# Performance work log

Hardware: AMD Instinct MI355X
Metric: run time of the kernel (lower is better)

The kernel has to match this reference:

```python
import jax, jax.numpy as jnp
import numpy as np

NHEAD = 16


def setup_inputs() -> dict:
    key = jax.random.key(0)
    ks = jax.random.split(key, 9)
    d = 1024
    scale = 0.03  # keep projected q,k in a sane range (like trained weights)
    return {
        "x": jax.random.normal(ks[0], (4, 4096, d), jnp.float32),
        "wq": jax.random.normal(ks[1], (d, d), jnp.float32) * scale,
        "bq": jax.random.normal(ks[2], (d,), jnp.float32) * scale,
        "wk": jax.random.normal(ks[3], (d, d), jnp.float32) * scale,
        "bk": jax.random.normal(ks[4], (d,), jnp.float32) * scale,
        "wv": jax.random.normal(ks[5], (d, d), jnp.float32) * scale,
        "bv": jax.random.normal(ks[6], (d,), jnp.float32) * scale,
        "wo": jax.random.normal(ks[7], (d, d), jnp.float32) * scale,
        "bo": jax.random.normal(ks[8], (d,), jnp.float32) * scale,
        "window_size": 128,
    }


def reference(x, wq, bq, wk, bk, wv, bv, wo, bo, window_size):
    B, S, D = x.shape
    H = NHEAD
    Dh = D // H
    w = int(window_size)

    def proj(wm, b):
        # [B,S,D] -> [B,H,S,Dh]
        return (x @ wm.T + b).reshape(B, S, H, Dh).transpose(0, 2, 1, 3)

    q = proj(wq, bq)
    k = proj(wk, bk)
    v = proj(wv, bv)

    # Pad K/V along seq so offset slices are static-size [B,H,S,Dh].
    Kp = jnp.pad(k, ((0, 0), (0, 0), (w, w), (0, 0)))
    Vp = jnp.pad(v, ((0, 0), (0, 0), (w, w), (0, 0)))
    pos = jnp.arange(S)
    inv_sqrt = np.float32(1.0 / np.sqrt(Dh))

    # Faithful to the Triton kernel: a sequential scan over window offsets with a
    # RUNNING max but NO rescaling of the accumulators (the kernel's exact math).
    def step(carry, t):
        m, o_acc, t_acc = carry
        kj = jax.lax.dynamic_slice_in_dim(Kp, t, S, axis=2)  # key at offset t-w
        vj = jax.lax.dynamic_slice_in_dim(Vp, t, S, axis=2)
        s = jnp.einsum("bhsd,bhsd->bhs", q, kj) * inv_sqrt
        j = pos + t - w
        valid = (j >= 0) & (j < S)  # [S], broadcasts over [B,H,S]
        m_new = jnp.where(valid, jnp.maximum(m, s), m)
        p = jnp.exp(jnp.where(valid, s - m_new, -jnp.inf))  # 0 where invalid
        return (m_new, o_acc + p[..., None] * vj, t_acc + p), None

    init = (
        jnp.full((B, H, S), -jnp.inf, dtype=x.dtype),
        jnp.zeros((B, H, S, Dh), dtype=x.dtype),
        jnp.zeros((B, H, S), dtype=x.dtype),
    )
    (m, o_acc, t_acc), _ = jax.lax.scan(step, init, jnp.arange(2 * w + 1))
    o = o_acc / t_acc[..., None]  # [B,H,S,Dh]
    out = o.transpose(0, 2, 1, 3).reshape(B, S, D)
    return out @ wo.T + bo
```

## Files before the change

### kernel.cpp

```cpp
#include <hip/hip_runtime.h>
#include <math.h>

#define S_LEN  4096
#define BATCH  4
#define DMODEL 1024
#define NHEADS 16
#define DHEAD  64
#define WIN    128

typedef _Float16 half8   __attribute__((ext_vector_type(8)));
typedef _Float16 half4_t __attribute__((ext_vector_type(4)));
typedef float    floatx4 __attribute__((ext_vector_type(4)));

__device__ __forceinline__ void gload16(const void* g, void* l) {
    __builtin_amdgcn_global_load_lds(
        (const __attribute__((address_space(1))) void*)g,
        (__attribute__((address_space(3))) void*)l, 16, 0, 0);
}

__global__ __launch_bounds__(256)
void cvt5_f32_f16(const float4* __restrict__ x,  half4_t* __restrict__ xo, int n4x,
                  const float4* __restrict__ w0, const float4* __restrict__ w1,
                  const float4* __restrict__ w2, const float4* __restrict__ w3,
                  half4_t* __restrict__ o0, half4_t* __restrict__ o1,
                  half4_t* __restrict__ o2, half4_t* __restrict__ o3, int n4w) {
    const int y = blockIdx.y;
    const float4* in  = y == 0 ? x  : (y == 1 ? w0 : (y == 2 ? w1 : (y == 3 ? w2 : w3)));
    half4_t*      out = y == 0 ? xo : (y == 1 ? o0 : (y == 2 ? o1 : (y == 3 ? o2 : o3)));
    const int n4 = y == 0 ? n4x : n4w;
    for (int i = blockIdx.x * blockDim.x + threadIdx.x; i < n4;
         i += gridDim.x * blockDim.x) {
        const float4 a = in[i];
        half4_t h;
        h[0] = (_Float16)a.x; h[1] = (_Float16)a.y;
        h[2] = (_Float16)a.z; h[3] = (_Float16)a.w;
        out[i] = h;
    }
}

template<int MODE, int NTN>
__global__ __launch_bounds__(512)
void gemm8p(const _Float16* __restrict__ A, const _Float16* __restrict__ W,
            const float* __restrict__ B0, const float* __restrict__ B1,
            const float* __restrict__ B2, void* __restrict__ out_base)
{
    constexpr int K  = DMODEL;
    constexpr int nt = K / 64;
    const int bid  = blockIdx.x;
    const int nwg8 = (64 * NTN) >> 3;
    const int swz  = (bid & 7) * nwg8 + (bid >> 3);
    const int i0   = (swz / NTN) * 256;
    const int n0   = (swz % NTN) * 256;

    __shared__ _Float16 As[4][128 * 64];
    __shared__ _Float16 Bs[4][128 * 64];

    const int tid  = threadIdx.x;
    const int lane = tid & 63;
    const int wid  = tid >> 6;
    const int wr   = wid >> 2;
    const int wc   = wid & 3;
    const int fr   = lane & 15;
    const int fh   = lane >> 4;
    const int sw8  = fr & 7;
    const int ok0  = ((fh) ^ sw8) * 8;
    const int ok1  = ((4 + fh) ^ sw8) * 8;
    const int arow = (wr * 16 + fr) * 64;
    const int brow = (wc * 16 + fr) * 64;

    const int srow = tid >> 3;
    const int ssw  = ((tid & 7) ^ (srow & 7)) << 3;
    const _Float16* baseA = A + (size_t)(i0 + srow) * K + ssw;
    const _Float16* baseB = W + (size_t)(n0 + srow) * K + ssw;
    const int ldso = tid * 8;

    floatx4 acc[8][4];
    #pragma unroll
    for (int mi = 0; mi < 8; ++mi)
        #pragma unroll
        for (int ni = 0; ni < 4; ++ni) acc[mi][ni] = (floatx4)0.f;

    half8 a_lo[4][2], a_hi[4][2], b_lo[2][2], b_hi[2][2];

#define ST_A(TT, H)                                                          \
    do {                                                                     \
        _Float16* d_ = &As[(((TT) & 1) << 1) | (H)][ldso];                   \
        const _Float16* s_ = baseA + (size_t)((H) * 128) * K + (TT) * 64;    \
        gload16(s_, d_);                                                     \
        gload16(s_ + (size_t)64 * K, d_ + 4096);                             \
    } while (0)
#define ST_B(TT, H)                                                          \
    do {                                                                     \
        _Float16* d_ = &Bs[(((TT) & 1) << 1) | (H)][ldso];                   \
        const _Float16* s_ = baseB + (size_t)((H) * 128) * K + (TT) * 64;    \
        gload16(s_, d_);                                                     \
        gload16(s_ + (size_t)64 * K, d_ + 4096);                             \
    } while (0)
#define RD_A(DST, DB, H)                                                     \
    _Pragma("unroll")                                                        \
    for (int mi = 0; mi < 4; ++mi) {                                         \
        DST[mi][0] = *(const half8*)&As[(DB) | (H)][arow + mi * 2048 + ok0]; \
        DST[mi][1] = *(const half8*)&As[(DB) | (H)][arow + mi * 2048 + ok1]; \
    }
#define RD_B(DST, DB, H)                                                     \
    _Pragma("unroll")                                                        \
    for (int ni = 0; ni < 2; ++ni) {                                         \
        DST[ni][0] = *(const half8*)&Bs[(DB) | (H)][brow + ni * 4096 + ok0]; \
        DST[ni][1] = *(const half8*)&Bs[(DB) | (H)][brow + ni * 4096 + ok1]; \
    }
#define MFMA16(MB, NB, AA, BB)                                               \
    __builtin_amdgcn_s_setprio(1);                                           \
    _Pragma("unroll")                                                        \
    for (int kc = 0; kc < 2; ++kc)                                           \
        _Pragma("unroll")                                                    \
        for (int mi = 0; mi < 4; ++mi)                                       \
            _Pragma("unroll")                                                \
            for (int ni = 0; ni < 2; ++ni)                                   \
                acc[MB + mi][NB + ni] = __builtin_amdgcn_mfma_f32_16x16x32_f16( \
                    AA[mi][kc], BB[ni][kc], acc[MB + mi][NB + ni], 0, 0, 0); \
    __builtin_amdgcn_s_setprio(0);
#define PHEND                                                                \
    asm volatile("s_waitcnt lgkmcnt(0)" ::: "memory");                       \
    __builtin_amdgcn_sched_barrier(0);                                       \
    __builtin_amdgcn_s_barrier();

    ST_A(0, 0); ST_B(0, 0); ST_B(0, 1); ST_A(0, 1);
    ST_A(1, 0); ST_B(1, 1); ST_A(1, 1); ST_B(1, 0);
    asm volatile("s_waitcnt vmcnt(8)" ::: "memory");
    __builtin_amdgcn_sched_barrier(0);
    __builtin_amdgcn_s_barrier();
    RD_A(a_lo, 0, 0); RD_B(b_lo, 0, 0);
    asm volatile("s_waitcnt lgkmcnt(0)" ::: "memory");
    __builtin_amdgcn_sched_barrier(0);

    for (int t = 0; t < nt; ++t) {
        const int d2 = (t & 1) << 1;
        const bool st = (t + 2) < nt;
        RD_B(b_hi, d2, 1);
        MFMA16(0, 0, a_lo, b_lo);
        PHEND;
        RD_A(a_hi, d2, 1);
        if (st) { ST_B(t + 2, 1); ST_A(t + 2, 0); }
        MFMA16(0, 2, a_lo, b_hi);
        PHEND;
        if (st) ST_A(t + 2, 1);
        MFMA16(4, 2, a_hi, b_hi);
        PHEND;
        if (st) ST_B(t + 2, 0);
        MFMA16(4, 0, a_hi, b_lo);
        if (st) {
            asm volatile("s_waitcnt vmcnt(8)" ::: "memory");
        } else if (t + 1 < nt) {
            asm volatile("s_waitcnt vmcnt(0)" ::: "memory");
        }
        __builtin_amdgcn_sched_barrier(0);
        __builtin_amdgcn_s_barrier();
        if (t + 1 < nt) {
            const int dn = ((t + 1) & 1) << 1;
            RD_A(a_lo, dn, 0); RD_B(b_lo, dn, 0);
            asm volatile("s_waitcnt lgkmcnt(0)" ::: "memory");
            __builtin_amdgcn_sched_barrier(0);
        }
    }
#undef ST_A
#undef ST_B
#undef RD_A
#undef RD_B
#undef MFMA16
#undef PHEND

    const int z  = (MODE == 0) ? (n0 >> 10) : 0;
    const float* bz = (MODE == 1) ? B0 : (z == 0 ? B0 : (z == 1 ? B1 : B2));

    #pragma unroll
    for (int ni = 0; ni < 4; ++ni) {
        const int gc   = n0 + ni * 64 + wc * 16 + fr;
        const int gcol = gc & (DMODEL - 1);
        const float bv = bz[gcol];
        #pragma unroll
        for (int mi = 0; mi < 8; ++mi) {
            const int gr = i0 + mi * 32 + wr * 16 + fh * 4;
            const floatx4 v = acc[mi][ni];
            if (MODE == 0) {
                _Float16* outh = (_Float16*)out_base
                               + (size_t)z * ((size_t)16384 * DMODEL);
                const int bb = gr >> 12;
                const int sp = gr & (S_LEN - 1);
                const int hh = gcol >> 6;
                const int dh = gcol & 63;
                if (z < 2) {
                    #pragma unroll
                    for (int r = 0; r < 4; ++r)
                        outh[((((size_t)(bb * NHEADS + hh)) * S_LEN + sp + r) << 6) + dh] =
                            (_Float16)(v[r] + bv);
                } else {
                    half4_t hv;
                    hv[0] = (_Float16)(v[0] + bv); hv[1] = (_Float16)(v[1] + bv);
                    hv[2] = (_Float16)(v[2] + bv); hv[3] = (_Float16)(v[3] + bv);
                    *(half4_t*)&outh[(((size_t)(bb * NHEADS + hh)) * DHEAD + dh) * S_LEN + sp] = hv;
                }
            } else {
                float* out = (float*)out_base;
                #pragma unroll
                for (int r = 0; r < 4; ++r)
                    out[(size_t)(gr + r) * DMODEL + gcol] = v[r] + bv;
            }
        }
    }
}

__global__ __launch_bounds__(256)
void attn_mfma(const _Float16* __restrict__ qh_, const _Float16* __restrict__ kh_,
               const _Float16* __restrict__ vth_, _Float16* __restrict__ o)
{
    __shared__ __align__(16) _Float16 Qs[64 * 64];
    __shared__ __align__(16) _Float16 Ks[64 * 64];
    __shared__ __align__(16) _Float16 Vt[64 * 64];
    __shared__ __align__(16) float    SP[64 * 68];
    __shared__ __align__(16) _Float16 P16[64 * 64];
    __shared__ float CM[64 * 4];
    __shared__ float TSs[64 * 4];
    __shared__ float Mq[64];
    __shared__ float Tq[64];

    const int tid   = threadIdx.x;
    const int lane  = tid & 63;
    const int w     = tid >> 6;
    const int qbase = blockIdx.x * 64;
    const int head  = blockIdx.y, b = blockIdx.z;
    const size_t bh = (size_t)(b * NHEADS + head);

    const _Float16* qg = qh_  + bh * (size_t)(S_LEN * DHEAD);
    const _Float16* kg = kh_  + bh * (size_t)(S_LEN * DHEAD);
    const _Float16* vg = vth_ + bh * (size_t)(DHEAD * S_LEN);

    const int fr = lane & 15;
    const int fh = lane >> 4;

    #pragma unroll
    for (int rep = 0; rep < 2; ++rep) {
        const int c = tid + 256 * rep;
        const int row = c >> 3, sll = c & 7;
        gload16(qg + (size_t)(qbase + row) * 64 + (size_t)((sll ^ (row & 7)) * 8),
                Qs + (size_t)c * 8);
    }
    if (tid < 64) { Mq[tid] = -INFINITY; Tq[tid] = 0.f; }

    floatx4 Oacc[4];
    #pragma unroll
    for (int ni = 0; ni < 4; ++ni) Oacc[ni] = (floatx4)0.f;

    for (int c = 0; c < 5; ++c) {
        const int jlo = qbase - WIN + c * 64;
        if (jlo < 0 || jlo >= S_LEN) continue;
        const int base_rel = jlo - qbase + WIN;

        __syncthreads();

        #pragma unroll
        for (int rep = 0; rep < 2; ++rep) {
            const int cc = tid + 256 * rep;
            const int row = cc >> 3, sll = cc & 7;
            gload16(kg + (size_t)(jlo + row) * 64 + (size_t)((sll ^ (row & 7)) * 8),
                    Ks + (size_t)cc * 8);
            gload16(vg + (size_t)row * S_LEN + jlo + (size_t)((sll ^ (row & 7)) * 8),
                    Vt + (size_t)cc * 8);
        }
        __syncthreads();

        {
            floatx4 acc[4];
            #pragma unroll
            for (int ni = 0; ni < 4; ++ni) acc[ni] = (floatx4)0.f;
            half8 a[2];
            #pragma unroll
            for (int kc = 0; kc < 2; ++kc) {
                const int row = 16 * w + fr;
                a[kc] = *(const half8*)&Qs[row * 64 + ((fh + 4 * kc) ^ (row & 7)) * 8];
            }
            #pragma unroll
            for (int ni = 0; ni < 4; ++ni)
                #pragma unroll
                for (int kc = 0; kc < 2; ++kc) {
                    const int tr = 16 * ni + fr;
                    half8 bf = *(const half8*)&Ks[tr * 64 + ((fh + 4 * kc) ^ (tr & 7)) * 8];
                    acc[ni] = __builtin_amdgcn_mfma_f32_16x16x32_f16(a[kc], bf, acc[ni], 0, 0, 0);
                }
            #pragma unroll
            for (int ni = 0; ni < 4; ++ni)
                #pragma unroll
                for (int r = 0; r < 4; ++r)
                    SP[(16 * w + 4 * fh + r) * 68 + fr + 16 * ni] = acc[ni][r] * 0.125f;
        }
        __syncthreads();

        const int sq = lane;
        float sv[16], run[16];
        {
            float m_run = -INFINITY;
            #pragma unroll
            for (int u = 0; u < 4; ++u) {
                const float4 s4 = *(const float4*)&SP[sq * 68 + w * 16 + 4 * u];
                const float se[4] = {s4.x, s4.y, s4.z, s4.w};
                #pragma unroll
                for (int e = 0; e < 4; ++e) {
                    const int i = 4 * u + e;
                    const int rel = base_rel + 16 * w + i - sq;
                    const bool valid = (rel >= 0) && (rel <= 2 * WIN);
                    const float s = valid ? se[e] : -INFINITY;
                    sv[i] = s;
                    m_run = fmaxf(m_run, s);
                    run[i] = m_run;
                }
            }
            CM[sq * 4 + w] = m_run;
        }
        __syncthreads();

        {
            float pre = Mq[sq];
            if (w > 0) pre = fmaxf(pre, CM[sq * 4 + 0]);
            if (w > 1) pre = fmaxf(pre, CM[sq * 4 + 1]);
            if (w > 2) pre = fmaxf(pre, CM[sq * 4 + 2]);
            float tl = 0.f;
            _Float16 pf[16];
            #pragma unroll
            for (int i = 0; i < 16; ++i) {
                const float wv = fmaxf(pre, run[i]);
                const float p = (sv[i] != -INFINITY) ? __expf(sv[i] - wv) : 0.f;
                tl += p;
                pf[i] = (_Float16)p;
            }
            TSs[sq * 4 + w] = tl;
            #pragma unroll
            for (int u = 0; u < 2; ++u) {
                half8 h8;
                #pragma unroll
                for (int e = 0; e < 8; ++e) h8[e] = pf[8 * u + e];
                *(half8*)&P16[sq * 64 + ((2 * w + u) ^ (sq & 7)) * 8] = h8;
            }
        }
        __syncthreads();

        if (tid < 64) {
            const float mm = fmaxf(fmaxf(CM[tid * 4 + 0], CM[tid * 4 + 1]),
                                   fmaxf(CM[tid * 4 + 2], CM[tid * 4 + 3]));
            Mq[tid] = fmaxf(Mq[tid], mm);
            Tq[tid] += TSs[tid * 4 + 0] + TSs[tid * 4 + 1] + TSs[tid * 4 + 2] + TSs[tid * 4 + 3];
        }

        {
            half8 pa[2];
            #pragma unroll
            for (int kc = 0; kc < 2; ++kc) {
                const int row = 16 * w + fr;
                pa[kc] = *(const half8*)&P16[row * 64 + ((fh + 4 * kc) ^ (row & 7)) * 8];
            }
            #pragma unroll
            for (int ni = 0; ni < 4; ++ni)
                #pragma unroll
                for (int kc = 0; kc < 2; ++kc) {
                    const int dr = 16 * ni + fr;
                    half8 bf = *(const half8*)&Vt[dr * 64 + ((fh + 4 * kc) ^ (dr & 7)) * 8];
                    Oacc[ni] = __builtin_amdgcn_mfma_f32_16x16x32_f16(pa[kc], bf, Oacc[ni], 0, 0, 0);
                }
        }
    }

    __syncthreads();

    #pragma unroll
    for (int ni = 0; ni < 4; ++ni)
        #pragma unroll
        for (int r = 0; r < 4; ++r) {
            const int q  = 16 * w + 4 * fh + r;
            const float inv = 1.0f / Tq[q];
            o[((size_t)(b * S_LEN + qbase + q) * NHEADS + head) * DHEAD + fr + 16 * ni] =
                (_Float16)(Oacc[ni][r] * inv);
        }
}

extern "C" void kernel_launch(void* const* d_in, const int* in_sizes, int n_in,
                              void* d_out, int out_size, void* d_ws, size_t ws_size,
                              hipStream_t stream) {
    const float* x  = (const float*)d_in[0];
    const float* wq = (const float*)d_in[1];
    const float* bq = (const float*)d_in[2];
    const float* wk = (const float*)d_in[3];
    const float* bk = (const float*)d_in[4];
    const float* wv = (const float*)d_in[5];
    const float* bv = (const float*)d_in[6];
    const float* wo = (const float*)d_in[7];
    const float* bo = (const float*)d_in[8];

    const size_t BUF = (size_t)BATCH * S_LEN * DMODEL;
    _Float16* xh  = (_Float16*)d_ws;
    _Float16* qh  = xh + BUF;
    _Float16* kh  = qh + BUF;
    _Float16* vth = kh + BUF;
    _Float16* oh  = vth + BUF;
    _Float16* wqh = oh + BUF;
    _Float16* wkh = wqh + DMODEL * DMODEL;
    _Float16* wvh = wkh + DMODEL * DMODEL;
    _Float16* woh = wvh + DMODEL * DMODEL;

    cvt5_f32_f16<<<dim3(512, 5), 256, 0, stream>>>(
        (const float4*)x, (half4_t*)xh, (int)(BUF / 4),
        (const float4*)wq, (const float4*)wk, (const float4*)wv, (const float4*)wo,
        (half4_t*)wqh, (half4_t*)wkh, (half4_t*)wvh, (half4_t*)woh,
        DMODEL * DMODEL / 4);

    gemm8p<0, 12><<<64 * 12, 512, 0, stream>>>(xh, wqh, bq, bk, bv, (void*)qh);

    dim3 gattn(S_LEN / 64, NHEADS, BATCH);
    attn_mfma<<<gattn, 256, 0, stream>>>(qh, kh, vth, oh);

    gemm8p<1, 4><<<64 * 4, 512, 0, stream>>>(oh, woh, bo, bo, bo, d_out);
}
```

Baseline: 257.1 us.

## Keep softmax row stats per wave via shuffles, drop block barriers

Reassigns the softmax stage so each wave handles only its own 16 query rows, with four lanes per row, and combines partial row maxima and sums through lane shuffles. Running max and denominator move from shared memory into registers. Three of the four block-wide barriers per key chunk become wave-local LDS waits. This removes cross-wave synchronisation and shared-memory traffic for the row statistics, at the cost of more shuffle instructions and a dependence on each wave touching only its own rows of SP and P16.

```diff
diff --git a/kernel.cpp b/kernel.cpp
--- a/kernel.cpp
+++ b/kernel.cpp
@@ -218,10 +218,7 @@
     __shared__ __align__(16) _Float16 Vt[64 * 64];
     __shared__ __align__(16) float    SP[64 * 68];
     __shared__ __align__(16) _Float16 P16[64 * 64];
-    __shared__ float CM[64 * 4];
-    __shared__ float TSs[64 * 4];
-    __shared__ float Mq[64];
-    __shared__ float Tq[64];
+    __shared__ float TqL[64];
 
     const int tid   = threadIdx.x;
     const int lane  = tid & 63;
@@ -234,8 +231,11 @@
     const _Float16* kg = kh_  + bh * (size_t)(S_LEN * DHEAD);
     const _Float16* vg = vth_ + bh * (size_t)(DHEAD * S_LEN);
 
-    const int fr = lane & 15;
-    const int fh = lane >> 4;
+    const int fr  = lane & 15;
+    const int fh  = lane >> 4;
+    const int sqt = 16 * w + (lane >> 2);
+    const int sg  = lane & 3;
+    const int gb  = lane & ~3;
 
     #pragma unroll
     for (int rep = 0; rep < 2; ++rep) {
@@ -244,7 +244,9 @@
         gload16(qg + (size_t)(qbase + row) * 64 + (size_t)((sll ^ (row & 7)) * 8),
                 Qs + (size_t)c * 8);
     }
-    if (tid < 64) { Mq[tid] = -INFINITY; Tq[tid] = 0.f; }
+
+    float mq = -INFINITY;
+    float tq = 0.f;
 
     floatx4 Oacc[4];
     #pragma unroll
@@ -292,20 +294,20 @@
                 for (int r = 0; r < 4; ++r)
                     SP[(16 * w + 4 * fh + r) * 68 + fr + 16 * ni] = acc[ni][r] * 0.125f;
         }
-        __syncthreads();
-
-        const int sq = lane;
-        float sv[16], run[16];
+        asm volatile("s_waitcnt lgkmcnt(0)" ::: "memory");
+        __builtin_amdgcn_sched_barrier(0);
+
         {
+            float sv[16], run[16];
             float m_run = -INFINITY;
             #pragma unroll
             for (int u = 0; u < 4; ++u) {
-                const float4 s4 = *(const float4*)&SP[sq * 68 + w * 16 + 4 * u];
+                const float4 s4 = *(const float4*)&SP[sqt * 68 + sg * 16 + 4 * u];
                 const float se[4] = {s4.x, s4.y, s4.z, s4.w};
                 #pragma unroll
                 for (int e = 0; e < 4; ++e) {
                     const int i = 4 * u + e;
-                    const int rel = base_rel + 16 * w + i - sq;
+                    const int rel = base_rel + sg * 16 + i - sqt;
                     const bool valid = (rel >= 0) && (rel <= 2 * WIN);
                     const float s = valid ? se[e] : -INFINITY;
                     sv[i] = s;
@@ -313,41 +315,41 @@
                     run[i] = m_run;
                 }
             }
-            CM[sq * 4 + w] = m_run;
-        }
-        __syncthreads();
-
-        {
-            float pre = Mq[sq];
-            if (w > 0) pre = fmaxf(pre, CM[sq * 4 + 0]);
-            if (w > 1) pre = fmaxf(pre, CM[sq * 4 + 1]);
-            if (w > 2) pre = fmaxf(pre, CM[sq * 4 + 2]);
+            const float cm = m_run;
+            const float c0 = __shfl(cm, gb + 0);
+            const float c1 = __shfl(cm, gb + 1);
+            const float c2 = __shfl(cm, gb + 2);
+            const float c3 = __shfl(cm, gb + 3);
+            float pre = mq;
+            if (sg > 0) pre = fmaxf(pre, c0);
+            if (sg > 1) pre = fmaxf(pre, c1);
+            if (sg > 2) pre = fmaxf(pre, c2);
+
             float tl = 0.f;
             _Float16 pf[16];
             #pragma unroll
             for (int i = 0; i < 16; ++i) {
-                const float wv = fmaxf(pre, run[i]);
-                const float p = (sv[i] != -INFINITY) ? __expf(sv[i] - wv) : 0.f;
+                const float wm = fmaxf(pre, run[i]);
+                const float p = (sv[i] != -INFINITY) ? __expf(sv[i] - wm) : 0.f;
                 tl += p;
                 pf[i] = (_Float16)p;
             }
-            TSs[sq * 4 + w] = tl;
             #pragma unroll
             for (int u = 0; u < 2; ++u) {
                 half8 h8;
                 #pragma unroll
                 for (int e = 0; e < 8; ++e) h8[e] = pf[8 * u + e];
-                *(half8*)&P16[sq * 64 + ((2 * w + u) ^ (sq & 7)) * 8] = h8;
-            }
-        }
-        __syncthreads();
-
-        if (tid < 64) {
-            const float mm = fmaxf(fmaxf(CM[tid * 4 + 0], CM[tid * 4 + 1]),
-                                   fmaxf(CM[tid * 4 + 2], CM[tid * 4 + 3]));
-            Mq[tid] = fmaxf(Mq[tid], mm);
-            Tq[tid] += TSs[tid * 4 + 0] + TSs[tid * 4 + 1] + TSs[tid * 4 + 2] + TSs[tid * 4 + 3];
-        }
+                *(half8*)&P16[sqt * 64 + ((2 * sg + u) ^ (sqt & 7)) * 8] = h8;
+            }
+            const float t0 = __shfl(tl, gb + 0);
+            const float t1 = __shfl(tl, gb + 1);
+            const float t2 = __shfl(tl, gb + 2);
+            const float t3 = __shfl(tl, gb + 3);
+            tq += t0 + t1 + t2 + t3;
+            mq = fmaxf(mq, fmaxf(fmaxf(c0, c1), fmaxf(c2, c3)));
+        }
+        asm volatile("s_waitcnt lgkmcnt(0)" ::: "memory");
+        __builtin_amdgcn_sched_barrier(0);
 
         {
             half8 pa[2];
@@ -367,14 +369,16 @@
         }
     }
 
-    __syncthreads();
+    if (sg == 0) TqL[sqt] = tq;
+    asm volatile("s_waitcnt lgkmcnt(0)" ::: "memory");
+    __builtin_amdgcn_sched_barrier(0);
 
     #pragma unroll
     for (int ni = 0; ni < 4; ++ni)
         #pragma unroll
         for (int r = 0; r < 4; ++r) {
             const int q  = 16 * w + 4 * fh + r;
-            const float inv = 1.0f / Tq[q];
+            const float inv = 1.0f / TqL[q];
             o[((size_t)(b * S_LEN + qbase + q) * NHEADS + head) * DHEAD + fr + 16 * ni] =
                 (_Float16)(Oacc[ni][r] * inv);
         }
```

Result: faster. 250.8 us (-2.4%).
